# Kernel tuning notes

Hardware: AMD Instinct MI355X
Metric: run time of the kernel (lower is better)

The kernel has to match this reference:

```python
import math
import jax, jax.numpy as jnp
import numpy as np

NHEAD = 16
HEAD_DIM = 64
D_MODEL = 1024
B, T = 2, 4096


def setup_inputs() -> dict:
    key = jax.random.key(0)
    ks = jax.random.split(key, 9)
    HD = NHEAD * HEAD_DIM
    s_in = 1.0 / math.sqrt(D_MODEL)
    s_out = 1.0 / math.sqrt(HD)
    return {
        "x": jax.random.normal(ks[0], (B, T, D_MODEL), dtype=jnp.float32),
        "Wq": jax.random.normal(ks[1], (D_MODEL, HD), dtype=jnp.float32) * s_in,
        "bq": jnp.zeros((HD,), dtype=jnp.float32),
        "Wk": jax.random.normal(ks[2], (D_MODEL, HD), dtype=jnp.float32) * s_in,
        "bk": jnp.zeros((HD,), dtype=jnp.float32),
        "Wv": jax.random.normal(ks[3], (D_MODEL, HD), dtype=jnp.float32) * s_in,
        "bv": jnp.zeros((HD,), dtype=jnp.float32),
        "Wo": jax.random.normal(ks[4], (HD, D_MODEL), dtype=jnp.float32) * s_out,
        "bo": jnp.zeros((D_MODEL,), dtype=jnp.float32),
    }


def _cosformer(x, Wq, bq, Wk, bk, Wv, bv, Wo, bo):
    Bsz, Tlen, _ = x.shape
    H, dh = NHEAD, HEAD_DIM
    # projections -> [B, T, H, dh]
    Q = (x @ Wq + bq).reshape(Bsz, Tlen, H, dh)
    K = (x @ Wk + bk).reshape(Bsz, Tlen, H, dh)
    V = (x @ Wv + bv).reshape(Bsz, Tlen, H, dh)
    Qp = jax.nn.relu(Q)
    Kp = jax.nn.relu(K)
    # cosFormer position reweighting: angle_i = pi/(2M) * i, M = T
    angles = (math.pi / (2.0 * Tlen)) * jnp.arange(Tlen, dtype=jnp.float32)
    cosw = jnp.cos(angles)[None, :, None, None]
    sinw = jnp.sin(angles)[None, :, None, None]
    Qc, Qs = Qp * cosw, Qp * sinw
    Kc, Ks = Kp * cosw, Kp * sinw
    # scan over time with O(d^2) causal state instead of materializing (B,H,T,d,d)
    # reorder to time-major [T, B, H, dh]
    tm = lambda a: jnp.moveaxis(a, 1, 0)
    Qc, Qs, Kc, Ks, Vt = tm(Qc), tm(Qs), tm(Kc), tm(Ks), tm(V)

    S0 = jnp.zeros((Bsz, H, dh, dh), dtype=x.dtype)
    z0 = jnp.zeros((Bsz, H, dh), dtype=x.dtype)

    def step(carry, inp):
        S_cos, S_sin, z_cos, z_sin = carry
        qc, qs, kc, ks_, v = inp  # each [B, H, dh]
        S_cos = S_cos + kc[..., :, None] * v[..., None, :]
        S_sin = S_sin + ks_[..., :, None] * v[..., None, :]
        z_cos = z_cos + kc
        z_sin = z_sin + ks_
        num = jnp.einsum('bhi,bhij->bhj', qc, S_cos) + jnp.einsum('bhi,bhij->bhj', qs, S_sin)
        den = jnp.sum(qc * z_cos + qs * z_sin, axis=-1)
        den = jnp.maximum(den, 1e-6)[..., None]
        return (S_cos, S_sin, z_cos, z_sin), num / den

    _, out = jax.lax.scan(step, (S0, S0, z0, z0), (Qc, Qs, Kc, Ks, Vt))
    # out: [T, B, H, dh] -> [B, T, H*dh]
    out = jnp.moveaxis(out, 0, 1).reshape(Bsz, Tlen, H * dh)
    return out @ Wo + bo


def reference(x, Wq, bq, Wk, bk, Wv, bv, Wo, bo):
    return _cosformer(x, Wq, bq, Wk, bk, Wv, bv, Wo, bo)
```

## Files before the change

### kernel.cpp

```cpp
#include <hip/hip_runtime.h>

#define NTOK   8192
#define DM     1024
#define HD_    1024
#define TSEQ   4096
#define NCH    64
#define SROWS  72
#define SHALF  (SROWS*64)
#define SSTR   (2*SHALF)
#define ANG_STEP 3.8349519697141029e-4f

typedef _Float16 h8_t  __attribute__((ext_vector_type(8)));
typedef _Float16 h4_t  __attribute__((ext_vector_type(4)));
typedef float    f32x4 __attribute__((ext_vector_type(4)));

__device__ __forceinline__ void gload16(const void* g, void* l) {
    __builtin_amdgcn_global_load_lds(
        (const __attribute__((address_space(1))) void*)g,
        (__attribute__((address_space(3))) void*)l, 16, 0, 0);
}

__device__ __forceinline__ void gemm_core(
    const _Float16* __restrict__ A, const _Float16* __restrict__ Wt,
    const float* __restrict__ bias, int mode,
    _Float16* rows16, _Float16* tp16, float* rows32,
    _Float16 (*As)[32], _Float16 (*Bs)[32])
{
    const int tid = threadIdx.x;
    const int lane = tid & 63, w = tid >> 6;
    const int m_base = blockIdx.x * 128, n_base = blockIdx.y * 128;

    const int r0 = tid >> 2;
    const int cb0 = (tid & 3) << 4;
    const _Float16* ga = A  + (size_t)(m_base + r0) * DM + (cb0 >> 1);
    const _Float16* gb = Wt + (size_t)(n_base + r0) * DM + (cb0 >> 1);
    char* lA = (char*)As + w * 1024;
    char* lB = (char*)Bs + w * 1024;

    f32x4 acc[4][4];
#pragma unroll
    for (int i = 0; i < 4; ++i)
#pragma unroll
        for (int j = 0; j < 4; ++j) acc[i][j] = (f32x4){0.f, 0.f, 0.f, 0.f};

    const int wm = (w >> 1) * 64, wn = (w & 1) * 64;
    const int fr = lane & 15;
    const int fk = (lane >> 4) * 16;

    for (int kt = 0; kt < DM / 32; ++kt) {
        const int k0 = kt * 32;
        __syncthreads();
        gload16(ga + k0,           lA);
        gload16(ga + 64 * DM + k0, lA + 4096);
        gload16(gb + k0,           lB);
        gload16(gb + 64 * DM + k0, lB + 4096);
        __syncthreads();
        h8_t a[4], b[4];
#pragma unroll
        for (int i = 0; i < 4; ++i) {
            a[i] = *(const h8_t*)((const char*)&As[wm + i * 16 + fr][0] + fk);
            b[i] = *(const h8_t*)((const char*)&Bs[wn + i * 16 + fr][0] + fk);
        }
#pragma unroll
        for (int i = 0; i < 4; ++i)
#pragma unroll
            for (int j = 0; j < 4; ++j)
                acc[i][j] = __builtin_amdgcn_mfma_f32_16x16x32_f16(a[i], b[j], acc[i][j], 0, 0, 0);
    }

    const int cn = lane & 15, rm = (lane >> 4) * 4;
#pragma unroll
    for (int j = 0; j < 4; ++j) {
        const int col = n_base + wn + j * 16 + cn;
        const float bs = bias[col];
#pragma unroll
        for (int i = 0; i < 4; ++i) {
            const int m0 = m_base + wm + i * 16 + rm;
            if (mode == 3) {
#pragma unroll
                for (int r = 0; r < 4; ++r)
                    rows32[(size_t)(m0 + r) * HD_ + col] = acc[i][j][r] + bs;
            } else {
                float v[4];
#pragma unroll
                for (int r = 0; r < 4; ++r) {
                    v[r] = acc[i][j][r] + bs;
                    if (mode <= 1) v[r] = fmaxf(v[r], 0.f);
                }
                if (mode <= 1) {
#pragma unroll
                    for (int r = 0; r < 4; ++r)
                        rows16[(size_t)(m0 + r) * HD_ + col] = (_Float16)v[r];
                }
                if (mode >= 1) {
                    h4_t pk;
#pragma unroll
                    for (int r = 0; r < 4; ++r) pk[r] = (_Float16)v[r];
                    const int bb = m0 >> 12, t = m0 & 4095;
                    const int hh = col >> 6, dd = col & 63;
                    *(h4_t*)(tp16 + ((size_t)(bb * 16 + hh) * 64 + dd) * TSEQ + t) = pk;
                }
            }
        }
    }
}

__global__ __launch_bounds__(256) void gemm_qkv(
    const _Float16* __restrict__ Xh, const _Float16* __restrict__ WtQKV,
    const float* __restrict__ bq, const float* __restrict__ bk, const float* __restrict__ bv,
    _Float16* __restrict__ Qh, _Float16* __restrict__ Kh,
    _Float16* __restrict__ KT, _Float16* __restrict__ VT)
{
    __shared__ _Float16 As[128][32];
    __shared__ _Float16 Bs[128][32];
    const int z = blockIdx.z;
    const _Float16* Wt = WtQKV + (size_t)z * (DM * HD_);
    const float* bias = (z == 0) ? bq : (z == 1) ? bk : bv;
    _Float16* r16 = (z == 0) ? Qh : Kh;
    _Float16* t16 = (z == 1) ? KT : VT;
    gemm_core(Xh, Wt, bias, z, r16, t16, nullptr, As, Bs);
}

__global__ __launch_bounds__(256) void gemm_out(
    const _Float16* __restrict__ A, const _Float16* __restrict__ Wt,
    const float* __restrict__ bias, float* __restrict__ out)
{
    __shared__ _Float16 As[128][32];
    __shared__ _Float16 Bs[128][32];
    gemm_core(A, Wt, bias, 3, nullptr, nullptr, out, As, Bs);
}

__global__ __launch_bounds__(256) void conv_x_kernel(
    const float* __restrict__ x, _Float16* __restrict__ xh)
{
    const int i = blockIdx.x * 256 + threadIdx.x;
    float4 v = ((const float4*)x)[i];
    h4_t hv;
    hv[0] = (_Float16)v.x; hv[1] = (_Float16)v.y;
    hv[2] = (_Float16)v.z; hv[3] = (_Float16)v.w;
    ((h4_t*)xh)[i] = hv;
}

__global__ __launch_bounds__(256) void conv_wt4(
    const float* __restrict__ Wq, const float* __restrict__ Wk,
    const float* __restrict__ Wv, const float* __restrict__ Wo,
    _Float16* __restrict__ WtQKV, _Float16* __restrict__ WtO)
{
    __shared__ float t[32][33];
    const int z = blockIdx.z;
    const float* W = (z == 0) ? Wq : (z == 1) ? Wk : (z == 2) ? Wv : Wo;
    _Float16* Wt = (z < 3) ? WtQKV + (size_t)z * DM * HD_ : WtO;
    const int bx = blockIdx.x * 32, by = blockIdx.y * 32;
    const int tx = threadIdx.x, ty = threadIdx.y;
#pragma unroll
    for (int i = 0; i < 4; ++i)
        t[ty + 8 * i][tx] = W[(size_t)(by + ty + 8 * i) * HD_ + bx + tx];
    __syncthreads();
#pragma unroll
    for (int i = 0; i < 4; ++i)
        Wt[(size_t)(bx + ty + 8 * i) * DM + by + tx] = (_Float16)t[tx][ty + 8 * i];
}

__global__ __launch_bounds__(256) void chunk_sums(
    const _Float16* __restrict__ KT, const _Float16* __restrict__ VT,
    _Float16* __restrict__ states)
{
    __shared__ char sm[26880];
    _Float16* cwh = (_Float16*)(sm);
    _Float16* swh = (_Float16*)(sm + 128);
    #define CS_KC 256
    #define CS_KS 8448
    #define CS_VT 16640

    const int c = blockIdx.x, bh = blockIdx.y;
    const int tid = threadIdx.x, lane = tid & 63, w = tid >> 6;

    if (tid < 64) {
        float s_, c_;
        sincosf(ANG_STEP * (float)(c * 64 + tid), &s_, &c_);
        cwh[tid] = (_Float16)c_; swh[tid] = (_Float16)s_;
    }
    __syncthreads();

    const size_t ktb = (size_t)(bh * 64) * TSEQ + c * 64;
#pragma unroll
    for (int rnd = 0; rnd < 2; ++rnd) {
        int lin = rnd * 256 + tid;
        int r = lin >> 3, u = lin & 7;
        h8_t kv = *(const h8_t*)(KT + ktb + (size_t)r * TSEQ + u * 8);
        h8_t c8 = *(const h8_t*)&cwh[u * 8];
        h8_t s8 = *(const h8_t*)&swh[u * 8];
        int sb = (r * 128 + u * 16) ^ ((r & 7) << 4);
        *(h8_t*)(sm + CS_KC + sb) = kv * c8;
        *(h8_t*)(sm + CS_KS + sb) = kv * s8;
    }
    const _Float16* vtb = VT + (size_t)(bh * 64) * TSEQ + c * 64;
#pragma unroll
    for (int rnd = 0; rnd < 2; ++rnd) {
        int lin = rnd * 256 + tid;
        int r = lin >> 3, u = lin & 7;
        gload16(vtb + (size_t)r * TSEQ + (u ^ (r & 7)) * 8,
                sm + CS_VT + (rnd * 256 + w * 64) * 16);
    }
    if (tid < 8) {
        h8_t one;
#pragma unroll
        for (int e = 0; e < 8; ++e) one[e] = (_Float16)1.0f;
        *(h8_t*)(sm + CS_VT + 64 * 128 + tid * 16) = one;
    }
    __syncthreads();

    const int fr = lane & 15, rm = (lane >> 4) * 4;
    _Float16* stc = states + (size_t)(bh * NCH + c) * SSTR;

    for (int half = 0; half < 2; ++half) {
        const int ko = half ? CS_KS : CS_KC;
        f32x4 acc[4][5];
#pragma unroll
        for (int i = 0; i < 4; ++i)
#pragma unroll
            for (int j = 0; j < 5; ++j) acc[i][j] = (f32x4){0.f, 0.f, 0.f, 0.f};
#pragma unroll
        for (int ks = 0; ks < 2; ++ks) {
            const int fko = ks * 64 + (lane >> 4) * 16;
            h8_t af[4], bf[5];
#pragma unroll
            for (int i = 0; i < 4; ++i) {
                int row = i * 16 + fr;
                af[i] = *(const h8_t*)(sm + ko + ((row * 128 + fko) ^ ((row & 7) << 4)));
            }
#pragma unroll
            for (int j = 0; j < 5; ++j) {
                int row = j * 16 + fr;
                bf[j] = *(const h8_t*)(sm + CS_VT + ((row * 128 + fko) ^ ((row & 7) << 4)));
            }
#pragma unroll
            for (int i = 0; i < 4; ++i)
#pragma unroll
                for (int j = 0; j < 5; ++j)
                    acc[i][j] = __builtin_amdgcn_mfma_f32_16x16x32_f16(af[i], bf[j], acc[i][j], 0, 0, 0);
        }
        _Float16* dst = stc + half * SHALF;
#pragma unroll
        for (int j = 0; j < 5; ++j) {
            int n = j * 16 + fr;
#pragma unroll
            for (int i = 0; i < 4; ++i) {
                h4_t pk;
#pragma unroll
                for (int r = 0; r < 4; ++r) pk[r] = (_Float16)acc[i][j][r];
                if (n <= 64) *(h4_t*)(dst + (size_t)n * 64 + i * 16 + rm) = pk;
            }
        }
    }
}

__global__ __launch_bounds__(256) void scan_kernel(_Float16* __restrict__ states)
{
    const int e8 = blockIdx.x * 256 + threadIdx.x;
    if (e8 >= SSTR / 8) return;
    _Float16* p = states + (size_t)blockIdx.y * (NCH * (size_t)SSTR) + (size_t)e8 * 8;
    float run[8];
#pragma unroll
    for (int e = 0; e < 8; ++e) run[e] = 0.f;
    for (int c = 0; c < NCH; c += 4) {
        h8_t v0 = *(const h8_t*)(p + (size_t)(c + 0) * SSTR);
        h8_t v1 = *(const h8_t*)(p + (size_t)(c + 1) * SSTR);
        h8_t v2 = *(const h8_t*)(p + (size_t)(c + 2) * SSTR);
        h8_t v3 = *(const h8_t*)(p + (size_t)(c + 3) * SSTR);
        h8_t o0, o1, o2, o3;
#pragma unroll
        for (int e = 0; e < 8; ++e) {
            o0[e] = (_Float16)run[e]; run[e] += (float)v0[e];
            o1[e] = (_Float16)run[e]; run[e] += (float)v1[e];
            o2[e] = (_Float16)run[e]; run[e] += (float)v2[e];
            o3[e] = (_Float16)run[e]; run[e] += (float)v3[e];
        }
        *(h8_t*)(p + (size_t)(c + 0) * SSTR) = o0;
        *(h8_t*)(p + (size_t)(c + 1) * SSTR) = o1;
        *(h8_t*)(p + (size_t)(c + 2) * SSTR) = o2;
        *(h8_t*)(p + (size_t)(c + 3) * SSTR) = o3;
    }
}

__global__ __launch_bounds__(256) void attn_mfma(
    const _Float16* __restrict__ Qh, const _Float16* __restrict__ Kh,
    const _Float16* __restrict__ VT, const _Float16* __restrict__ states,
    _Float16* __restrict__ atth)
{
    __shared__ char sm[53248];
    float* cwf = (float*)(sm);
    float* swf = (float*)(sm + 256);
    _Float16* cwh = (_Float16*)(sm + 512);
    _Float16* swh = (_Float16*)(sm + 640);
    #define AT_Q 768
    #define AT_K 8960
    #define AT_A 17152
    #define AT_V 25344
    #define AT_C 33792
    #define AT_S 43008

    const int c = blockIdx.x, bh = blockIdx.y;
    const int b = bh >> 4, h = bh & 15;
    const int tid = threadIdx.x, lane = tid & 63, w = tid >> 6;
    const int tok0 = b * TSEQ + c * 64;

    if (tid < 64) {
        float s_, c_;
        sincosf(ANG_STEP * (float)(c * 64 + tid), &s_, &c_);
        cwf[tid] = c_; swf[tid] = s_;
        cwh[tid] = (_Float16)c_; swh[tid] = (_Float16)s_;
    }

    const _Float16* stb = states + (size_t)(bh * NCH + c) * SSTR;
#pragma unroll
    for (int rnd = 0; rnd < 2; ++rnd) {
        int lin = rnd * 256 + tid;
        int r = lin >> 3, u = lin & 7;
        int su = (u ^ (r & 7)) * 8;
        char* lb = sm + (rnd * 256 + w * 64) * 16;
        gload16(Qh + (size_t)(tok0 + r) * HD_ + h * 64 + su, lb + AT_Q);
        gload16(Kh + (size_t)(tok0 + r) * HD_ + h * 64 + su, lb + AT_K);
        gload16(VT + (size_t)(bh * 64 + r) * TSEQ + c * 64 + su, lb + AT_V);
    }
#pragma unroll
    for (int rnd = 0; rnd < 3; ++rnd) {
        if (rnd < 2 || tid < 64) {
            int lin = rnd * 256 + tid;
            int r = lin >> 3, u = lin & 7;
            int su = (u ^ (r & 7)) * 8;
            char* lb = sm + (rnd * 256 + w * 64) * 16;
            gload16(stb + (size_t)r * 64 + su, lb + AT_C);
            gload16(stb + SHALF + (size_t)r * 64 + su, lb + AT_S);
        }
    }
    if (tid < 8) {
        h8_t one;
#pragma unroll
        for (int e = 0; e < 8; ++e) one[e] = (_Float16)1.0f;
        *(h8_t*)(sm + AT_V + 64 * 128 + tid * 16) = one;
    }
    __syncthreads();

    const int fr = lane & 15;
    f32x4 dt[4][4];
#pragma unroll
    for (int i = 0; i < 4; ++i)
#pragma unroll
        for (int j = 0; j < 4; ++j) dt[i][j] = (f32x4){0.f, 0.f, 0.f, 0.f};
#pragma unroll
    for (int ks = 0; ks < 2; ++ks) {
        const int fko = ks * 64 + (lane >> 4) * 16;
        h8_t ak[4], bq[4];
#pragma unroll
        for (int i = 0; i < 4; ++i) {
            int row = i * 16 + fr;
            int sb = (row * 128 + fko) ^ ((row & 7) << 4);
            ak[i] = *(const h8_t*)(sm + AT_K + sb);
            bq[i] = *(const h8_t*)(sm + AT_Q + sb);
        }
#pragma unroll
        for (int i = 0; i < 4; ++i)
#pragma unroll
            for (int j = 0; j < 4; ++j)
                dt[i][j] = __builtin_amdgcn_mfma_f32_16x16x32_f16(ak[i], bq[j], dt[i][j], 0, 0, 0);
    }
    {
        const int sr0 = (lane >> 4) * 4;
#pragma unroll
        for (int j = 0; j < 4; ++j) {
            const int tt = j * 16 + fr;
            const float cwt = cwf[tt], swt = swf[tt];
#pragma unroll
            for (int i = 0; i < 4; ++i) {
                const int s0 = i * 16 + sr0;
                h4_t pk;
#pragma unroll
                for (int r = 0; r < 4; ++r) {
                    int s = s0 + r;
                    float f = cwt * cwf[s] + swt * swf[s];
                    float a = (s <= tt) ? dt[i][j][r] * f : 0.f;
                    pk[r] = (_Float16)a;
                }
                int sb = (tt * 128 + s0 * 2) ^ ((tt & 7) << 4);
                *(h4_t*)(sm + AT_A + sb) = pk;
            }
        }
    }
    __syncthreads();

    f32x4 o[4][5];
#pragma unroll
    for (int i = 0; i < 4; ++i)
#pragma unroll
        for (int j = 0; j < 5; ++j) o[i][j] = (f32x4){0.f, 0.f, 0.f, 0.f};
#pragma unroll
    for (int ks = 0; ks < 2; ++ks) {
        const int fko = ks * 64 + (lane >> 4) * 16;
        h8_t aa[4], aqc[4], aqs[4];
#pragma unroll
        for (int i = 0; i < 4; ++i) {
            int row = i * 16 + fr;
            int sb = (row * 128 + fko) ^ ((row & 7) << 4);
            aa[i] = *(const h8_t*)(sm + AT_A + sb);
            h8_t q8 = *(const h8_t*)(sm + AT_Q + sb);
            aqc[i] = q8 * cwh[row];
            aqs[i] = q8 * swh[row];
        }
#pragma unroll
        for (int j = 0; j < 5; ++j) {
            int row = j * 16 + fr;
            int sb = (row * 128 + fko) ^ ((row & 7) << 4);
            h8_t bv = *(const h8_t*)(sm + AT_V + sb);
            h8_t bc = *(const h8_t*)(sm + AT_C + sb);
            h8_t bs = *(const h8_t*)(sm + AT_S + sb);
#pragma unroll
            for (int i = 0; i < 4; ++i) {
                o[i][j] = __builtin_amdgcn_mfma_f32_16x16x32_f16(aa[i],  bv, o[i][j], 0, 0, 0);
                o[i][j] = __builtin_amdgcn_mfma_f32_16x16x32_f16(aqc[i], bc, o[i][j], 0, 0, 0);
                o[i][j] = __builtin_amdgcn_mfma_f32_16x16x32_f16(aqs[i], bs, o[i][j], 0, 0, 0);
            }
        }
    }
    char* Ce = sm + AT_K;
    const int rm = (lane >> 4) * 4;
#pragma unroll
    for (int i = 0; i < 4; ++i) {
        float rden[4];
#pragma unroll
        for (int r = 0; r < 4; ++r)
            rden[r] = 1.0f / fmaxf(__shfl(o[i][4][r], lane & 48), 1e-6f);
#pragma unroll
        for (int j = 0; j < 4; ++j) {
            const int col = j * 16 + fr;
#pragma unroll
            for (int r = 0; r < 4; ++r) {
                const int t = i * 16 + rm + r;
                const int byte = ((t << 7) + (col << 1)) ^ ((t & 7) << 4);
                *(_Float16*)(Ce + byte) = (_Float16)(o[i][j][r] * rden[r]);
            }
        }
    }
    __syncthreads();
#pragma unroll
    for (int p = 0; p < 2; ++p) {
        const int lin = p * 256 + tid;
        const int t = lin >> 3, d8 = lin & 7;
        h8_t v = *(const h8_t*)(Ce + (t << 7) + ((d8 ^ (t & 7)) << 4));
        *(h8_t*)(atth + (size_t)(tok0 + t) * HD_ + h * 64 + d8 * 8) = v;
    }
}

extern "C" void kernel_launch(void* const* d_in, const int* in_sizes, int n_in,
                              void* d_out, int out_size, void* d_ws, size_t ws_size,
                              hipStream_t stream)
{
    const float* x  = (const float*)d_in[0];
    const float* Wq = (const float*)d_in[1];
    const float* bq = (const float*)d_in[2];
    const float* Wk = (const float*)d_in[3];
    const float* bk = (const float*)d_in[4];
    const float* Wv = (const float*)d_in[5];
    const float* bv = (const float*)d_in[6];
    const float* Wo = (const float*)d_in[7];
    const float* bo = (const float*)d_in[8];
    float* out = (float*)d_out;

    _Float16* ws = (_Float16*)d_ws;
    _Float16* Xh     = ws;
    _Float16* WtQKV  = Xh + (size_t)NTOK * DM;
    _Float16* WtO    = WtQKV + 3 * (size_t)DM * HD_;
    _Float16* Qh     = WtO + (size_t)DM * HD_;
    _Float16* Kh     = Qh + (size_t)NTOK * HD_;
    _Float16* KT     = Kh + (size_t)NTOK * HD_;
    _Float16* VT     = KT + (size_t)NTOK * HD_;
    _Float16* atth   = VT + (size_t)NTOK * HD_;
    _Float16* states = atth + (size_t)NTOK * HD_;

    dim3 tb(256);
    hipLaunchKernelGGL(conv_x_kernel, dim3(NTOK * DM / 1024), tb, 0, stream, x, Xh);
    hipLaunchKernelGGL(conv_wt4, dim3(32, 32, 4), dim3(32, 8), 0, stream,
                       Wq, Wk, Wv, Wo, WtQKV, WtO);
    hipLaunchKernelGGL(gemm_qkv, dim3(64, 8, 3), tb, 0, stream,
                       Xh, WtQKV, bq, bk, bv, Qh, Kh, KT, VT);
    hipLaunchKernelGGL(chunk_sums, dim3(NCH, 32), tb, 0, stream, KT, VT, states);
    hipLaunchKernelGGL(scan_kernel, dim3(5, 32), tb, 0, stream, states);
    hipLaunchKernelGGL(attn_mfma, dim3(NCH, 32), tb, 0, stream, Qh, Kh, VT, states, atth);
    hipLaunchKernelGGL(gemm_out, dim3(64, 8), tb, 0, stream, atth, WtO, bo, out);
}
```

Measured before the change: 295.6 us.

## Split chunk-state and attention MFMA tiles across warps instead of redundant compute

New measurement: 262.7 us. 1.13x faster.

```diff
diff --git a/kernel.cpp b/kernel.cpp
--- a/kernel.cpp
+++ b/kernel.cpp
@@ -212,45 +212,35 @@
 
     const int fr = lane & 15, rm = (lane >> 4) * 4;
     _Float16* stc = states + (size_t)(bh * NCH + c) * SSTR;
+    const int rowA = w * 16 + fr;
 
     for (int half = 0; half < 2; ++half) {
         const int ko = half ? CS_KS : CS_KC;
-        f32x4 acc[4][5];
-#pragma unroll
-        for (int i = 0; i < 4; ++i)
-#pragma unroll
-            for (int j = 0; j < 5; ++j) acc[i][j] = (f32x4){0.f, 0.f, 0.f, 0.f};
+        f32x4 acc[5];
+#pragma unroll
+        for (int j = 0; j < 5; ++j) acc[j] = (f32x4){0.f, 0.f, 0.f, 0.f};
 #pragma unroll
         for (int ks = 0; ks < 2; ++ks) {
             const int fko = ks * 64 + (lane >> 4) * 16;
-            h8_t af[4], bf[5];
-#pragma unroll
-            for (int i = 0; i < 4; ++i) {
-                int row = i * 16 + fr;
-                af[i] = *(const h8_t*)(sm + ko + ((row * 128 + fko) ^ ((row & 7) << 4)));
-            }
+            h8_t af = *(const h8_t*)(sm + ko + ((rowA * 128 + fko) ^ ((rowA & 7) << 4)));
+            h8_t bf[5];
 #pragma unroll
             for (int j = 0; j < 5; ++j) {
                 int row = j * 16 + fr;
                 bf[j] = *(const h8_t*)(sm + CS_VT + ((row * 128 + fko) ^ ((row & 7) << 4)));
             }
 #pragma unroll
-            for (int i = 0; i < 4; ++i)
-#pragma unroll
-                for (int j = 0; j < 5; ++j)
-                    acc[i][j] = __builtin_amdgcn_mfma_f32_16x16x32_f16(af[i], bf[j], acc[i][j], 0, 0, 0);
+            for (int j = 0; j < 5; ++j)
+                acc[j] = __builtin_amdgcn_mfma_f32_16x16x32_f16(af, bf[j], acc[j], 0, 0, 0);
         }
         _Float16* dst = stc + half * SHALF;
 #pragma unroll
         for (int j = 0; j < 5; ++j) {
             int n = j * 16 + fr;
-#pragma unroll
-            for (int i = 0; i < 4; ++i) {
-                h4_t pk;
-#pragma unroll
-                for (int r = 0; r < 4; ++r) pk[r] = (_Float16)acc[i][j][r];
-                if (n <= 64) *(h4_t*)(dst + (size_t)n * 64 + i * 16 + rm) = pk;
-            }
+            h4_t pk;
+#pragma unroll
+            for (int r = 0; r < 4; ++r) pk[r] = (_Float16)acc[j][r];
+            if (n <= 64) *(h4_t*)(dst + (size_t)n * 64 + w * 16 + rm) = pk;
         }
     }
 }
@@ -343,70 +333,55 @@
     __syncthreads();
 
     const int fr = lane & 15;
-    f32x4 dt[4][4];
-#pragma unroll
-    for (int i = 0; i < 4; ++i)
-#pragma unroll
-        for (int j = 0; j < 4; ++j) dt[i][j] = (f32x4){0.f, 0.f, 0.f, 0.f};
+    const int ttw = w * 16 + fr;
+    f32x4 dt[4];
+#pragma unroll
+    for (int i = 0; i < 4; ++i) dt[i] = (f32x4){0.f, 0.f, 0.f, 0.f};
 #pragma unroll
     for (int ks = 0; ks < 2; ++ks) {
         const int fko = ks * 64 + (lane >> 4) * 16;
-        h8_t ak[4], bq[4];
+        h8_t bqw = *(const h8_t*)(sm + AT_Q + ((ttw * 128 + fko) ^ ((ttw & 7) << 4)));
+        h8_t ak[4];
 #pragma unroll
         for (int i = 0; i < 4; ++i) {
             int row = i * 16 + fr;
-            int sb = (row * 128 + fko) ^ ((row & 7) << 4);
-            ak[i] = *(const h8_t*)(sm + AT_K + sb);
-            bq[i] = *(const h8_t*)(sm + AT_Q + sb);
+            ak[i] = *(const h8_t*)(sm + AT_K + ((row * 128 + fko) ^ ((row & 7) << 4)));
         }
 #pragma unroll
         for (int i = 0; i < 4; ++i)
-#pragma unroll
-            for (int j = 0; j < 4; ++j)
-                dt[i][j] = __builtin_amdgcn_mfma_f32_16x16x32_f16(ak[i], bq[j], dt[i][j], 0, 0, 0);
+            dt[i] = __builtin_amdgcn_mfma_f32_16x16x32_f16(ak[i], bqw, dt[i], 0, 0, 0);
     }
     {
         const int sr0 = (lane >> 4) * 4;
-#pragma unroll
-        for (int j = 0; j < 4; ++j) {
-            const int tt = j * 16 + fr;
-            const float cwt = cwf[tt], swt = swf[tt];
-#pragma unroll
-            for (int i = 0; i < 4; ++i) {
-                const int s0 = i * 16 + sr0;
-                h4_t pk;
-#pragma unroll
-                for (int r = 0; r < 4; ++r) {
-                    int s = s0 + r;
-                    float f = cwt * cwf[s] + swt * swf[s];
-                    float a = (s <= tt) ? dt[i][j][r] * f : 0.f;
-                    pk[r] = (_Float16)a;
-                }
-                int sb = (tt * 128 + s0 * 2) ^ ((tt & 7) << 4);
-                *(h4_t*)(sm + AT_A + sb) = pk;
+        const float cwt = cwf[ttw], swt = swf[ttw];
+#pragma unroll
+        for (int i = 0; i < 4; ++i) {
+            const int s0 = i * 16 + sr0;
+            h4_t pk;
+#pragma unroll
+            for (int r = 0; r < 4; ++r) {
+                int s = s0 + r;
+                float f = cwt * cwf[s] + swt * swf[s];
+                float a = (s <= ttw) ? dt[i][r] * f : 0.f;
+                pk[r] = (_Float16)a;
             }
-        }
-    }
-    __syncthreads();
-
-    f32x4 o[4][5];
-#pragma unroll
-    for (int i = 0; i < 4; ++i)
-#pragma unroll
-        for (int j = 0; j < 5; ++j) o[i][j] = (f32x4){0.f, 0.f, 0.f, 0.f};
+            int sb = (ttw * 128 + s0 * 2) ^ ((ttw & 7) << 4);
+            *(h4_t*)(sm + AT_A + sb) = pk;
+        }
+    }
+    __syncthreads();
+
+    f32x4 o[5];
+#pragma unroll
+    for (int j = 0; j < 5; ++j) o[j] = (f32x4){0.f, 0.f, 0.f, 0.f};
 #pragma unroll
     for (int ks = 0; ks < 2; ++ks) {
         const int fko = ks * 64 + (lane >> 4) * 16;
-        h8_t aa[4], aqc[4], aqs[4];
-#pragma unroll
-        for (int i = 0; i < 4; ++i) {
-            int row = i * 16 + fr;
-            int sb = (row * 128 + fko) ^ ((row & 7) << 4);
-            aa[i] = *(const h8_t*)(sm + AT_A + sb);
-            h8_t q8 = *(const h8_t*)(sm + AT_Q + sb);
-            aqc[i] = q8 * cwh[row];
-            aqs[i] = q8 * swh[row];
-        }
+        const int sbA = (ttw * 128 + fko) ^ ((ttw & 7) << 4);
+        h8_t aa = *(const h8_t*)(sm + AT_A + sbA);
+        h8_t q8 = *(const h8_t*)(sm + AT_Q + sbA);
+        h8_t aqc = q8 * cwh[ttw];
+        h8_t aqs = q8 * swh[ttw];
 #pragma unroll
         for (int j = 0; j < 5; ++j) {
             int row = j * 16 + fr;
@@ -414,30 +389,26 @@
             h8_t bv = *(const h8_t*)(sm + AT_V + sb);
             h8_t bc = *(const h8_t*)(sm + AT_C + sb);
             h8_t bs = *(const h8_t*)(sm + AT_S + sb);
-#pragma unroll
-            for (int i = 0; i < 4; ++i) {
-                o[i][j] = __builtin_amdgcn_mfma_f32_16x16x32_f16(aa[i],  bv, o[i][j], 0, 0, 0);
-                o[i][j] = __builtin_amdgcn_mfma_f32_16x16x32_f16(aqc[i], bc, o[i][j], 0, 0, 0);
-                o[i][j] = __builtin_amdgcn_mfma_f32_16x16x32_f16(aqs[i], bs, o[i][j], 0, 0, 0);
-            }
+            o[j] = __builtin_amdgcn_mfma_f32_16x16x32_f16(aa,  bv, o[j], 0, 0, 0);
+            o[j] = __builtin_amdgcn_mfma_f32_16x16x32_f16(aqc, bc, o[j], 0, 0, 0);
+            o[j] = __builtin_amdgcn_mfma_f32_16x16x32_f16(aqs, bs, o[j], 0, 0, 0);
         }
     }
     char* Ce = sm + AT_K;
     const int rm = (lane >> 4) * 4;
-#pragma unroll
-    for (int i = 0; i < 4; ++i) {
+    {
         float rden[4];
 #pragma unroll
         for (int r = 0; r < 4; ++r)
-            rden[r] = 1.0f / fmaxf(__shfl(o[i][4][r], lane & 48), 1e-6f);
+            rden[r] = 1.0f / fmaxf(__shfl(o[4][r], lane & 48), 1e-6f);
 #pragma unroll
         for (int j = 0; j < 4; ++j) {
             const int col = j * 16 + fr;
 #pragma unroll
             for (int r = 0; r < 4; ++r) {
-                const int t = i * 16 + rm + r;
+                const int t = w * 16 + rm + r;
                 const int byte = ((t << 7) + (col << 1)) ^ ((t & 7) << 4);
-                *(_Float16*)(Ce + byte) = (_Float16)(o[i][j][r] * rden[r]);
+                *(_Float16*)(Ce + byte) = (_Float16)(o[j][r] * rden[r]);
             }
         }
     }
```
